# Kernel optimization log

Measured on AMD Instinct MI355X. Metric: run time of the kernel, lower is better.

## Reference

```python
import jax, jax.numpy as jnp
import numpy as np
import math

NEG = -1000000.0

def setup_inputs() -> dict:
    key = jax.random.key(0)
    k1, k2, k3, k4 = jax.random.split(key, 4)
    B, S, D = 64, 1024, 64
    query = jax.random.normal(k1, (B, S, D), dtype=jnp.float32)
    key_t = jax.random.normal(k2, (B, S, D), dtype=jnp.float32)
    value = jax.random.normal(k3, (B, S, D), dtype=jnp.float32)
    valid_lens = jax.random.randint(k4, (B,), 1, S + 1, dtype=jnp.int32)
    return {"query": query, "key": key_t, "value": value, "valid_lens": valid_lens}

def reference(query, key, value, valid_lens):
    # query/key/value: [B, S, D]; valid_lens: [B]
    d = query.shape[-1]
    scores = jnp.einsum('bqd,bkd->bqk', query, key) / math.sqrt(d)
    Sk = key.shape[1]
    # 1D valid_lens -> same mask for every query row (repeat_interleave semantics)
    mask = jnp.arange(Sk)[None, None, :] < valid_lens[:, None, None]  # [B,1,Sk]
    scores = jnp.where(mask, scores, NEG)
    weights = jax.nn.softmax(scores, axis=-1)
    # dropout p=0.0 -> identity
    return jnp.einsum('bqk,bkd->bqd', weights, value)
```

## Files before the change

### kernel.cpp

```cpp
#include <hip/hip_runtime.h>
#include <hip/hip_bf16.h>
#include <cstdint>


typedef __attribute__((ext_vector_type(8))) short short8;
typedef __attribute__((ext_vector_type(4))) short short4v;
typedef __attribute__((ext_vector_type(4))) float f32x4;

#define B_   64
#define S_   1024
#define D_   64
#define BQ   64
#define BK   64
#define KPAD 72

__device__ __forceinline__ f32x4 mfma16(short4v a, short4v b, f32x4 c) {
    return __builtin_amdgcn_mfma_f32_16x16x16bf16_1k(a, b, c, 0, 0, 0);
}

__device__ __forceinline__ uint32_t pk2(float a, float b) {
    float2 t; t.x = a; t.y = b;
    union { __hip_bfloat162 h; uint32_t u; } c;
    c.h = __float22bfloat162_rn(t);
    return c.u;
}

__global__ __launch_bounds__(256, 4)
void attn_fwd(const float* __restrict__ Q, const float* __restrict__ K,
              const float* __restrict__ V, const int* __restrict__ VL,
              float* __restrict__ Out) {
    __shared__ __align__(16) unsigned short lK [BK * KPAD];
    __shared__ __align__(16) unsigned short lVt[D_ * 64];

    const int tid  = threadIdx.x;
    const int wave = tid >> 6;
    const int lane = tid & 63;
    const int col  = lane & 15;
    const int quad = lane >> 4;

    const int bid  = blockIdx.x;
    const int b    = (bid & 7) * 8 + (bid >> 7);
    const int q0   = ((bid >> 3) & 15) * BQ;
    const int vlen = VL[b];
    const int ntiles = (vlen + BK - 1) / BK;

    const int T  = tid >> 4;
    const int m  = tid & 15;
    const int Tl = T & 3;
    const int cb = T >> 2;
    const int dcs = m >> 1;
    const int sws = ((dcs & 1) << 2) | (dcs >> 1);

    const float* Kb = K + (size_t)b * S_ * D_ + 4 * m;
    const float* Vb = V + (size_t)b * S_ * D_ + 4 * m;

    float4 kr[4], vr[4];
    #pragma unroll
    for (int j = 0; j < 4; ++j) {
        const int row = 2 * T + (j >> 1) * 32 + (j & 1);
        kr[j] = *(const float4*)(Kb + (size_t)row * D_);
        vr[j] = *(const float4*)(Vb + (size_t)row * D_);
    }

    short8 qa[2];
    {
        const int qrow = q0 + wave * 16 + col;
        const float* qp = Q + ((size_t)b * S_ + qrow) * D_ + quad * 8;
        #pragma unroll
        for (int c = 0; c < 2; ++c) {
            float4 x0 = *(const float4*)(qp + c * 32);
            float4 x1 = *(const float4*)(qp + c * 32 + 4);
            union { uint32_t u[4]; short8 s; } qq;
            qq.u[0] = pk2(x0.x, x0.y);
            qq.u[1] = pk2(x0.z, x0.w);
            qq.u[2] = pk2(x1.x, x1.y);
            qq.u[3] = pk2(x1.z, x1.w);
            qa[c] = qq.s;
        }
    }

    f32x4 ofrag[4];
    #pragma unroll
    for (int dt = 0; dt < 4; ++dt) ofrag[dt] = (f32x4){0.f, 0.f, 0.f, 0.f};
    float lsum = 0.f;

    const float cexp = 0.18033688011112042f;
    const int sws_v = (((col >> 1) & 1) << 2) | (col >> 2);

    for (int kt = 0; kt < ntiles; ++kt) {
        const int kbase = kt * BK;

        __syncthreads();

        #pragma unroll
        for (int j = 0; j < 4; ++j) {
            const int row = 2 * T + (j >> 1) * 32 + (j & 1);
            uint2 kv;
            kv.x = pk2(kr[j].x, kr[j].y);
            kv.y = pk2(kr[j].z, kr[j].w);
            *(uint2*)&lK[row * KPAD + 4 * m] = kv;
        }
        #pragma unroll
        for (int i = 0; i < 2; ++i) {
            const int p = (cb + 4 * i) ^ sws;
            unsigned short* base = &lVt[p * 8 + 2 * Tl];
            const float4 va = vr[2 * i], vb2 = vr[2 * i + 1];
            *(uint32_t*)&base[(4 * m + 0) * 64] = pk2(va.x, vb2.x);
            *(uint32_t*)&base[(4 * m + 1) * 64] = pk2(va.y, vb2.y);
            *(uint32_t*)&base[(4 * m + 2) * 64] = pk2(va.z, vb2.z);
            *(uint32_t*)&base[(4 * m + 3) * 64] = pk2(va.w, vb2.w);
        }

        __syncthreads();

        if (kt + 1 < ntiles) {
            const size_t off = (size_t)(kt + 1) * BK * D_;
            #pragma unroll
            for (int j = 0; j < 4; ++j) {
                const int row = 2 * T + (j >> 1) * 32 + (j & 1);
                kr[j] = *(const float4*)(Kb + off + (size_t)row * D_);
                vr[j] = *(const float4*)(Vb + off + (size_t)row * D_);
            }
        }

        f32x4 sfrag[4];
        #pragma unroll
        for (int ct = 0; ct < 4; ++ct) {
            f32x4 acc = (f32x4){0.f, 0.f, 0.f, 0.f};
            #pragma unroll
            for (int c = 0; c < 2; ++c) {
                short8 kf = *(const short8*)&lK[(ct * 16 + col) * KPAD + c * 32 + quad * 8];
                acc = __builtin_amdgcn_mfma_f32_16x16x32_bf16(kf, qa[c], acc, 0, 0, 0);
            }
            sfrag[ct] = acc;
        }

        short4v pb[4];
        if (kbase + BK <= vlen) {
            #pragma unroll
            for (int ct = 0; ct < 4; ++ct) {
                float e0 = __builtin_amdgcn_exp2f(sfrag[ct][0] * cexp);
                float e1 = __builtin_amdgcn_exp2f(sfrag[ct][1] * cexp);
                float e2 = __builtin_amdgcn_exp2f(sfrag[ct][2] * cexp);
                float e3 = __builtin_amdgcn_exp2f(sfrag[ct][3] * cexp);
                lsum += (e0 + e1) + (e2 + e3);
                union { uint32_t u[2]; short4v s; } pp;
                pp.u[0] = pk2(e0, e1);
                pp.u[1] = pk2(e2, e3);
                pb[ct] = pp.s;
            }
        } else {
            #pragma unroll
            for (int ct = 0; ct < 4; ++ct) {
                const int kv0 = kbase + ct * 16 + quad * 4;
                float e[4];
                #pragma unroll
                for (int rr = 0; rr < 4; ++rr) {
                    e[rr] = (kv0 + rr < vlen)
                          ? __builtin_amdgcn_exp2f(sfrag[ct][rr] * cexp) : 0.0f;
                    lsum += e[rr];
                }
                union { uint32_t u[2]; short4v s; } pp;
                pp.u[0] = pk2(e[0], e[1]);
                pp.u[1] = pk2(e[2], e[3]);
                pb[ct] = pp.s;
            }
        }

        #pragma unroll
        for (int ct = 0; ct < 4; ++ct) {
            const int K0 = ct * 16 + quad * 4;
            const int p  = (((K0 >> 3) & 3) + 4 * (K0 >> 5)) ^ sws_v;
            const int o8 = K0 & 7;
            #pragma unroll
            for (int dt = 0; dt < 4; ++dt) {
                short4v va = *(const short4v*)&lVt[(4 * col + dt) * 64 + p * 8 + o8];
                ofrag[dt] = mfma16(va, pb[ct], ofrag[dt]);
            }
        }
    }

    float sred = lsum;
    sred += __shfl_xor(sred, 16, 64);
    sred += __shfl_xor(sred, 32, 64);
    const float inv = 1.0f / sred;
    float* op = Out + ((size_t)b * S_ + q0 + wave * 16 + col) * D_ + 16 * quad;
    #pragma unroll
    for (int reg = 0; reg < 4; ++reg) {
        float4 o;
        o.x = ofrag[0][reg] * inv;
        o.y = ofrag[1][reg] * inv;
        o.z = ofrag[2][reg] * inv;
        o.w = ofrag[3][reg] * inv;
        *(float4*)(op + 4 * reg) = o;
    }
}

extern "C" void kernel_launch(void* const* d_in, const int* in_sizes, int n_in,
                              void* d_out, int out_size, void* d_ws, size_t ws_size,
                              hipStream_t stream) {
    const float* Q  = (const float*)d_in[0];
    const float* K  = (const float*)d_in[1];
    const float* V  = (const float*)d_in[2];
    const int*   VL = (const int*)d_in[3];
    float* Out = (float*)d_out;
    dim3 grid(B_ * (S_ / BQ));
    attn_fwd<<<grid, 256, 0, stream>>>(Q, K, V, VL, Out);
}
```

Measured before the change: 117.8 us.

## Use persistent blocks with atomic work queue, LPT batch ordering, and split-K waves

Replaces the fixed grid with 512 persistent 512-thread blocks that pull work items from a global atomic counter. Items are ordered by descending valid length so the longest batches are scheduled first. Within a block, pairs of waves split each 64-key tile into two 32-key halves, and their partial outputs and row sums are merged through shared memory at the end. This targets load imbalance from variable valid lengths, at the cost of an extra memset, atomics, barriers per item, and a shared-memory reduction.

```diff
diff --git a/kernel.cpp b/kernel.cpp
--- a/kernel.cpp
+++ b/kernel.cpp
@@ -7,12 +7,12 @@
 typedef __attribute__((ext_vector_type(4))) short short4v;
 typedef __attribute__((ext_vector_type(4))) float f32x4;
 
-#define B_   64
-#define S_   1024
-#define D_   64
-#define BQ   64
-#define BK   64
-#define KPAD 72
+#define B_     64
+#define S_     1024
+#define D_     64
+#define BK     64
+#define KPAD   72
+#define NITEMS 1024
 
 __device__ __forceinline__ f32x4 mfma16(short4v a, short4v b, f32x4 c) {
     return __builtin_amdgcn_mfma_f32_16x16x16bf16_1k(a, b, c, 0, 0, 0);
@@ -25,24 +25,26 @@
     return c.u;
 }
 
-__global__ __launch_bounds__(256, 4)
+__global__ __launch_bounds__(512, 4)
 void attn_fwd(const float* __restrict__ Q, const float* __restrict__ K,
               const float* __restrict__ V, const int* __restrict__ VL,
-              float* __restrict__ Out) {
-    __shared__ __align__(16) unsigned short lK [BK * KPAD];
-    __shared__ __align__(16) unsigned short lVt[D_ * 64];
+              float* __restrict__ Out, int* __restrict__ ws) {
+    __shared__ __align__(16) unsigned char smem[17408];
+    unsigned short* lK  = (unsigned short*)smem;
+    unsigned short* lVt = (unsigned short*)(smem + 9216);
+    float*          obuf = (float*)smem;
+    __shared__ float lL[64];
+    __shared__ int  sRank[64];
+    __shared__ int  sVlen[64];
+    __shared__ int  sItem;
 
     const int tid  = threadIdx.x;
     const int wave = tid >> 6;
     const int lane = tid & 63;
     const int col  = lane & 15;
     const int quad = lane >> 4;
-
-    const int bid  = blockIdx.x;
-    const int b    = (bid & 7) * 8 + (bid >> 7);
-    const int q0   = ((bid >> 3) & 15) * BQ;
-    const int vlen = VL[b];
-    const int ntiles = (vlen + BK - 1) / BK;
+    const int qg   = wave >> 1;
+    const int wk   = wave & 1;
 
     const int T  = tid >> 4;
     const int m  = tid & 15;
@@ -50,149 +52,191 @@
     const int cb = T >> 2;
     const int dcs = m >> 1;
     const int sws = ((dcs & 1) << 2) | (dcs >> 1);
-
-    const float* Kb = K + (size_t)b * S_ * D_ + 4 * m;
-    const float* Vb = V + (size_t)b * S_ * D_ + 4 * m;
-
-    float4 kr[4], vr[4];
-    #pragma unroll
-    for (int j = 0; j < 4; ++j) {
-        const int row = 2 * T + (j >> 1) * 32 + (j & 1);
-        kr[j] = *(const float4*)(Kb + (size_t)row * D_);
-        vr[j] = *(const float4*)(Vb + (size_t)row * D_);
+    const int sws_v = (((col >> 1) & 1) << 2) | (col >> 2);
+
+    if (tid < 64) {
+        const int myv = VL[tid];
+        int r = 0;
+        #pragma unroll 1
+        for (int j = 0; j < 64; ++j) {
+            const int vj = __shfl(myv, j, 64);
+            r += (vj > myv) || (vj == myv && j < tid);
+        }
+        sRank[r] = tid;
+        sVlen[tid] = myv;
     }
 
-    short8 qa[2];
-    {
-        const int qrow = q0 + wave * 16 + col;
-        const float* qp = Q + ((size_t)b * S_ + qrow) * D_ + quad * 8;
+    const float cexp = 0.18033688011112042f;
+
+    while (true) {
+        __syncthreads();
+        if (tid == 0) sItem = atomicAdd(ws, 1);
+        __syncthreads();
+        const int it = sItem;
+        if (it >= NITEMS) break;
+
+        const int b    = sRank[it >> 4];
+        const int q0   = (it & 15) * 64;
+        const int vlen = sVlen[b];
+        const int ntiles = (vlen + BK - 1) / BK;
+
+        const float* Kb = K + (size_t)b * S_ * D_ + 4 * m;
+        const float* Vb = V + (size_t)b * S_ * D_ + 4 * m;
+
+        float4 kr[2], vr[2];
         #pragma unroll
-        for (int c = 0; c < 2; ++c) {
-            float4 x0 = *(const float4*)(qp + c * 32);
-            float4 x1 = *(const float4*)(qp + c * 32 + 4);
-            union { uint32_t u[4]; short8 s; } qq;
-            qq.u[0] = pk2(x0.x, x0.y);
-            qq.u[1] = pk2(x0.z, x0.w);
-            qq.u[2] = pk2(x1.x, x1.y);
-            qq.u[3] = pk2(x1.z, x1.w);
-            qa[c] = qq.s;
-        }
-    }
-
-    f32x4 ofrag[4];
-    #pragma unroll
-    for (int dt = 0; dt < 4; ++dt) ofrag[dt] = (f32x4){0.f, 0.f, 0.f, 0.f};
-    float lsum = 0.f;
-
-    const float cexp = 0.18033688011112042f;
-    const int sws_v = (((col >> 1) & 1) << 2) | (col >> 2);
-
-    for (int kt = 0; kt < ntiles; ++kt) {
-        const int kbase = kt * BK;
-
-        __syncthreads();
-
+        for (int j = 0; j < 2; ++j) {
+            const int row = 2 * T + j;
+            kr[j] = *(const float4*)(Kb + (size_t)row * D_);
+            vr[j] = *(const float4*)(Vb + (size_t)row * D_);
+        }
+
+        short8 qa[2];
+        {
+            const float* qp = Q + ((size_t)b * S_ + q0 + qg * 16 + col) * D_ + quad * 8;
+            #pragma unroll
+            for (int c = 0; c < 2; ++c) {
+                float4 x0 = *(const float4*)(qp + c * 32);
+                float4 x1 = *(const float4*)(qp + c * 32 + 4);
+                union { uint32_t u[4]; short8 s; } qq;
+                qq.u[0] = pk2(x0.x, x0.y);
+                qq.u[1] = pk2(x0.z, x0.w);
+                qq.u[2] = pk2(x1.x, x1.y);
+                qq.u[3] = pk2(x1.z, x1.w);
+                qa[c] = qq.s;
+            }
+        }
+
+        f32x4 ofrag[4];
         #pragma unroll
-        for (int j = 0; j < 4; ++j) {
-            const int row = 2 * T + (j >> 1) * 32 + (j & 1);
-            uint2 kv;
-            kv.x = pk2(kr[j].x, kr[j].y);
-            kv.y = pk2(kr[j].z, kr[j].w);
-            *(uint2*)&lK[row * KPAD + 4 * m] = kv;
-        }
-        #pragma unroll
-        for (int i = 0; i < 2; ++i) {
-            const int p = (cb + 4 * i) ^ sws;
-            unsigned short* base = &lVt[p * 8 + 2 * Tl];
-            const float4 va = vr[2 * i], vb2 = vr[2 * i + 1];
-            *(uint32_t*)&base[(4 * m + 0) * 64] = pk2(va.x, vb2.x);
-            *(uint32_t*)&base[(4 * m + 1) * 64] = pk2(va.y, vb2.y);
-            *(uint32_t*)&base[(4 * m + 2) * 64] = pk2(va.z, vb2.z);
-            *(uint32_t*)&base[(4 * m + 3) * 64] = pk2(va.w, vb2.w);
-        }
-
-        __syncthreads();
-
-        if (kt + 1 < ntiles) {
-            const size_t off = (size_t)(kt + 1) * BK * D_;
-            #pragma unroll
-            for (int j = 0; j < 4; ++j) {
-                const int row = 2 * T + (j >> 1) * 32 + (j & 1);
-                kr[j] = *(const float4*)(Kb + off + (size_t)row * D_);
-                vr[j] = *(const float4*)(Vb + off + (size_t)row * D_);
-            }
-        }
-
-        f32x4 sfrag[4];
-        #pragma unroll
-        for (int ct = 0; ct < 4; ++ct) {
-            f32x4 acc = (f32x4){0.f, 0.f, 0.f, 0.f};
-            #pragma unroll
-            for (int c = 0; c < 2; ++c) {
-                short8 kf = *(const short8*)&lK[(ct * 16 + col) * KPAD + c * 32 + quad * 8];
-                acc = __builtin_amdgcn_mfma_f32_16x16x32_bf16(kf, qa[c], acc, 0, 0, 0);
-            }
-            sfrag[ct] = acc;
-        }
-
-        short4v pb[4];
-        if (kbase + BK <= vlen) {
-            #pragma unroll
-            for (int ct = 0; ct < 4; ++ct) {
-                float e0 = __builtin_amdgcn_exp2f(sfrag[ct][0] * cexp);
-                float e1 = __builtin_amdgcn_exp2f(sfrag[ct][1] * cexp);
-                float e2 = __builtin_amdgcn_exp2f(sfrag[ct][2] * cexp);
-                float e3 = __builtin_amdgcn_exp2f(sfrag[ct][3] * cexp);
-                lsum += (e0 + e1) + (e2 + e3);
-                union { uint32_t u[2]; short4v s; } pp;
-                pp.u[0] = pk2(e0, e1);
-                pp.u[1] = pk2(e2, e3);
-                pb[ct] = pp.s;
-            }
-        } else {
-            #pragma unroll
-            for (int ct = 0; ct < 4; ++ct) {
-                const int kv0 = kbase + ct * 16 + quad * 4;
-                float e[4];
+        for (int dt = 0; dt < 4; ++dt) ofrag[dt] = (f32x4){0.f, 0.f, 0.f, 0.f};
+        float lsum = 0.f;
+
+        #pragma unroll 1
+        for (int kt = 0; kt < ntiles; ++kt) {
+            const int kbase = kt * BK;
+
+            __syncthreads();
+
+            #pragma unroll
+            for (int j = 0; j < 2; ++j) {
+                uint2 kv;
+                kv.x = pk2(kr[j].x, kr[j].y);
+                kv.y = pk2(kr[j].z, kr[j].w);
+                *(uint2*)&lK[(2 * T + j) * KPAD + 4 * m] = kv;
+            }
+            {
+                const int p = cb ^ sws;
+                unsigned short* base = &lVt[p * 8 + 2 * Tl];
+                *(uint32_t*)&base[(4 * m + 0) * 64] = pk2(vr[0].x, vr[1].x);
+                *(uint32_t*)&base[(4 * m + 1) * 64] = pk2(vr[0].y, vr[1].y);
+                *(uint32_t*)&base[(4 * m + 2) * 64] = pk2(vr[0].z, vr[1].z);
+                *(uint32_t*)&base[(4 * m + 3) * 64] = pk2(vr[0].w, vr[1].w);
+            }
+
+            __syncthreads();
+
+            if (kt + 1 < ntiles) {
+                const size_t off = (size_t)(kt + 1) * BK * D_;
                 #pragma unroll
-                for (int rr = 0; rr < 4; ++rr) {
-                    e[rr] = (kv0 + rr < vlen)
-                          ? __builtin_amdgcn_exp2f(sfrag[ct][rr] * cexp) : 0.0f;
-                    lsum += e[rr];
-                }
-                union { uint32_t u[2]; short4v s; } pp;
-                pp.u[0] = pk2(e[0], e[1]);
-                pp.u[1] = pk2(e[2], e[3]);
-                pb[ct] = pp.s;
-            }
-        }
-
-        #pragma unroll
-        for (int ct = 0; ct < 4; ++ct) {
-            const int K0 = ct * 16 + quad * 4;
-            const int p  = (((K0 >> 3) & 3) + 4 * (K0 >> 5)) ^ sws_v;
-            const int o8 = K0 & 7;
-            #pragma unroll
-            for (int dt = 0; dt < 4; ++dt) {
-                short4v va = *(const short4v*)&lVt[(4 * col + dt) * 64 + p * 8 + o8];
-                ofrag[dt] = mfma16(va, pb[ct], ofrag[dt]);
-            }
-        }
-    }
-
-    float sred = lsum;
-    sred += __shfl_xor(sred, 16, 64);
-    sred += __shfl_xor(sred, 32, 64);
-    const float inv = 1.0f / sred;
-    float* op = Out + ((size_t)b * S_ + q0 + wave * 16 + col) * D_ + 16 * quad;
-    #pragma unroll
-    for (int reg = 0; reg < 4; ++reg) {
-        float4 o;
-        o.x = ofrag[0][reg] * inv;
-        o.y = ofrag[1][reg] * inv;
-        o.z = ofrag[2][reg] * inv;
-        o.w = ofrag[3][reg] * inv;
-        *(float4*)(op + 4 * reg) = o;
+                for (int j = 0; j < 2; ++j) {
+                    const int row = 2 * T + j;
+                    kr[j] = *(const float4*)(Kb + off + (size_t)row * D_);
+                    vr[j] = *(const float4*)(Vb + off + (size_t)row * D_);
+                }
+            }
+
+            const int kv_lo = kbase + 32 * wk;
+            if (kv_lo < vlen) {
+                f32x4 sfrag[2];
+                #pragma unroll
+                for (int ct = 0; ct < 2; ++ct) {
+                    f32x4 acc = (f32x4){0.f, 0.f, 0.f, 0.f};
+                    #pragma unroll
+                    for (int c = 0; c < 2; ++c) {
+                        short8 kf = *(const short8*)&lK[(32 * wk + ct * 16 + col) * KPAD + c * 32 + quad * 8];
+                        acc = __builtin_amdgcn_mfma_f32_16x16x32_bf16(kf, qa[c], acc, 0, 0, 0);
+                    }
+                    sfrag[ct] = acc;
+                }
+
+                short4v pb[2];
+                if (kv_lo + 32 <= vlen) {
+                    #pragma unroll
+                    for (int ct = 0; ct < 2; ++ct) {
+                        float e0 = __builtin_amdgcn_exp2f(sfrag[ct][0] * cexp);
+                        float e1 = __builtin_amdgcn_exp2f(sfrag[ct][1] * cexp);
+                        float e2 = __builtin_amdgcn_exp2f(sfrag[ct][2] * cexp);
+                        float e3 = __builtin_amdgcn_exp2f(sfrag[ct][3] * cexp);
+                        lsum += (e0 + e1) + (e2 + e3);
+                        union { uint32_t u[2]; short4v s; } pp;
+                        pp.u[0] = pk2(e0, e1);
+                        pp.u[1] = pk2(e2, e3);
+                        pb[ct] = pp.s;
+                    }
+                } else {
+                    #pragma unroll
+                    for (int ct = 0; ct < 2; ++ct) {
+                        const int kv0 = kv_lo + ct * 16 + quad * 4;
+                        float e[4];
+                        #pragma unroll
+                        for (int rr = 0; rr < 4; ++rr) {
+                            e[rr] = (kv0 + rr < vlen)
+                                  ? __builtin_amdgcn_exp2f(sfrag[ct][rr] * cexp) : 0.0f;
+                            lsum += e[rr];
+                        }
+                        union { uint32_t u[2]; short4v s; } pp;
+                        pp.u[0] = pk2(e[0], e[1]);
+                        pp.u[1] = pk2(e[2], e[3]);
+                        pb[ct] = pp.s;
+                    }
+                }
+
+                #pragma unroll
+                for (int ct = 0; ct < 2; ++ct) {
+                    const int K0 = 32 * wk + ct * 16 + quad * 4;
+                    const int p  = (((K0 >> 3) & 3) + 4 * (K0 >> 5)) ^ sws_v;
+                    const int o8 = K0 & 7;
+                    #pragma unroll
+                    for (int dt = 0; dt < 4; ++dt) {
+                        short4v va = *(const short4v*)&lVt[(4 * col + dt) * 64 + p * 8 + o8];
+                        ofrag[dt] = mfma16(va, pb[ct], ofrag[dt]);
+                    }
+                }
+            }
+        }
+
+        lsum += __shfl_xor(lsum, 16, 64);
+        lsum += __shfl_xor(lsum, 32, 64);
+
+        __syncthreads();
+        if (wk == 1) {
+            #pragma unroll
+            for (int reg = 0; reg < 4; ++reg) {
+                float4 t;
+                t.x = ofrag[0][reg];
+                t.y = ofrag[1][reg];
+                t.z = ofrag[2][reg];
+                t.w = ofrag[3][reg];
+                *(float4*)&obuf[(qg * 16 + col) * 68 + 16 * quad + 4 * reg] = t;
+            }
+            if (quad == 0) lL[qg * 16 + col] = lsum;
+        }
+        __syncthreads();
+        if (wk == 0) {
+            const float linv = 1.0f / (lsum + lL[qg * 16 + col]);
+            float* op = Out + ((size_t)b * S_ + q0 + qg * 16 + col) * D_ + 16 * quad;
+            #pragma unroll
+            for (int reg = 0; reg < 4; ++reg) {
+                float4 pA = *(const float4*)&obuf[(qg * 16 + col) * 68 + 16 * quad + 4 * reg];
+                float4 o;
+                o.x = (ofrag[0][reg] + pA.x) * linv;
+                o.y = (ofrag[1][reg] + pA.y) * linv;
+                o.z = (ofrag[2][reg] + pA.z) * linv;
+                o.w = (ofrag[3][reg] + pA.w) * linv;
+                *(float4*)(op + 4 * reg) = o;
+            }
+        }
     }
 }
 
@@ -204,6 +248,7 @@
     const float* V  = (const float*)d_in[2];
     const int*   VL = (const int*)d_in[3];
     float* Out = (float*)d_out;
-    dim3 grid(B_ * (S_ / BQ));
-    attn_fwd<<<grid, 256, 0, stream>>>(Q, K, V, VL, Out);
-}
+    hipMemsetAsync(d_ws, 0, 4, stream);
+    dim3 grid(512);
+    attn_fwd<<<grid, 512, 0, stream>>>(Q, K, V, VL, Out, (int*)d_ws);
+}
```

Result: slower. 121.8 us (+3.4%).
